# Kernel tuning notes

Hardware: AMD Instinct MI355X
Metric: run time of the kernel (lower is better)

The kernel has to match this reference:

```python
import jax, jax.numpy as jnp
import numpy as np

TEMPERATURE = 0.1  # matches init kwarg


def _l2_normalize(x):
    # tf.math.l2_normalize along axis=1
    return x / jnp.sqrt(jnp.sum(x * x, axis=1, keepdims=True))


def _nearest_neighbour(p, queue):
    # brute-force top-1 retrieval: [B,D] @ [D,Q] -> argmax -> gather
    sims = p @ queue.T                      # [B, Q]
    nn = queue[jnp.argmax(sims, axis=1)]    # [B, D]
    return p + jax.lax.stop_gradient(nn - p)


def setup_inputs() -> dict:
    key = jax.random.key(0)
    k1, k2, k3 = jax.random.split(key, 3)
    B, Q, D = 4096, 32768, 128
    return {
        "projections_1": jax.random.normal(k1, (B, D), dtype=jnp.float32),
        "projections_2": jax.random.normal(k2, (B, D), dtype=jnp.float32),
        "feature_queue": _l2_normalize(jax.random.normal(k3, (Q, D), dtype=jnp.float32)),
    }


def reference(projections_1, projections_2, feature_queue):
    p1 = _l2_normalize(projections_1)
    p2 = _l2_normalize(projections_2)
    n1 = _nearest_neighbour(p1, feature_queue)
    n2 = _nearest_neighbour(p2, feature_queue)
    t = TEMPERATURE
    s_1_2_1 = (n1 @ p2.T) / t   # [B, B]
    s_1_2_2 = (p2 @ n1.T) / t
    s_2_1_1 = (n2 @ p1.T) / t
    s_2_1_2 = (p1 @ n2.T) / t
    logits = jnp.concatenate([s_1_2_1, s_1_2_2, s_2_1_1, s_2_1_2], axis=0)  # [4B, B]
    B = p1.shape[0]
    labels = jnp.tile(jnp.arange(B), 4)  # [4B]
    log_probs = jax.nn.log_softmax(logits, axis=1)
    # sparse categorical crossentropy per row (from_logits=True)
    loss = -jnp.take_along_axis(log_probs, labels[:, None], axis=1)[:, 0]
    return loss
```

## Files before the change

kernel.cpp:

```cpp
#include <hip/hip_runtime.h>
#include <math.h>


#define B_N 4096
#define D_N 128
#define NP 8192
#define NTILE 512
#define INV_T 10.0f
#define C1F (10.0f * 1.4426950408889634f)
#define C2F (16.0f * 1.4426950408889634f)
#define W_WIN 8e-3f

typedef _Float16 half8 __attribute__((ext_vector_type(8)));
typedef __fp16 fp16x2 __attribute__((ext_vector_type(2)));
typedef float f32x4 __attribute__((ext_vector_type(4)));
union H8 { half8 v; fp16x2 h2[4]; };

#define OFF_PH 0u
#define OFF_QH 2097152u
#define OFF_NH 10485760u
#define OFF_TV 12582912u
#define OFF_RM1 20971520u
#define OFF_RM 21233664u
#define OFF_KEY 21266432u
#define OFF_DG 21331968u
#define OFF_SP 21364736u

__device__ __forceinline__ void gload16(const void* g, void* l) {
  __builtin_amdgcn_global_load_lds((const __attribute__((address_space(1))) void*)g,
                                   (__attribute__((address_space(3))) void*)l, 16, 0, 0);
}

__global__ __launch_bounds__(256) void k_normalize(const float* __restrict__ in1,
                                                   const float* __restrict__ in2,
                                                   _Float16* __restrict__ Ph) {
  int t = threadIdx.x, w = t >> 6, l = t & 63;
  int g = blockIdx.x * 4 + w;
  int view = g >> 12, row = g & (B_N - 1);
  const float* src = (view ? in2 : in1) + (size_t)row * D_N;
  float2 v = *(const float2*)(src + 2 * l);
  float ss = fmaf(v.x, v.x, v.y * v.y);
#pragma unroll
  for (int m = 1; m < 64; m <<= 1) ss += __shfl_xor(ss, m);
  float rn = 1.0f / sqrtf(ss);
  *(fp16x2*)(Ph + (size_t)g * D_N + 2 * l) = __builtin_amdgcn_cvt_pkrtz(v.x * rn, v.y * rn);
}

__global__ __launch_bounds__(256) void k_qcvt(const float* __restrict__ src,
                                              _Float16* __restrict__ dst) {
  int i = blockIdx.x * 256 + threadIdx.x;
  const float* s = src + (size_t)i * 8;
  float4 x = *(const float4*)s;
  float4 y = *(const float4*)(s + 4);
  H8 h;
  h.h2[0] = __builtin_amdgcn_cvt_pkrtz(x.x, x.y);
  h.h2[1] = __builtin_amdgcn_cvt_pkrtz(x.z, x.w);
  h.h2[2] = __builtin_amdgcn_cvt_pkrtz(y.x, y.y);
  h.h2[3] = __builtin_amdgcn_cvt_pkrtz(y.z, y.w);
  *(half8*)(dst + (size_t)i * 8) = h.v;
}

#define STAGE128(MAT, RB, BUF)                                                 \
  {                                                                            \
    _Pragma("unroll") for (int j = 0; j < 8; ++j) {                            \
      int ch = w * 8 + j;                                                      \
      int r = (ch << 2) + l4;                                                  \
      gload16(MAT + (((RB) + r) << 7) + ((l15 ^ (r & 7)) << 3),                \
              (char*)(&sm[BUF][0]) + (ch << 10));                              \
    }                                                                          \
  }

__global__ __launch_bounds__(256, 2) void k_nn(const _Float16* __restrict__ Qh,
                                               const _Float16* __restrict__ Ph,
                                               _Float16* __restrict__ tv) {
  __shared__ _Float16 sm[2][16384];
  int bid = blockIdx.x;
  int qc = (bid & 7) | ((bid >> 9) << 3);
  int pb = (bid >> 3) & 63;
  int t = threadIdx.x, l = t & 63, w = t >> 6;
  int wq = w >> 1, wp = w & 1, l15 = l & 15, l4 = l >> 4;
  half8 Pf4[4][4];
  const _Float16* pbase = Ph + (size_t)(pb * 128 + wp * 64 + l15) * D_N + l4 * 8;
#pragma unroll
  for (int tj = 0; tj < 4; ++tj)
#pragma unroll
    for (int ks = 0; ks < 4; ++ks)
      Pf4[tj][ks] = *(const half8*)(pbase + (size_t)tj * 16 * D_N + ks * 32);
  const size_t qrow0 = (size_t)qc * 2048;
  int tidb = qc * 32;
  int pcol = pb * 128 + wp * 64 + l15;
  STAGE128(Qh, qrow0, 0)
#pragma unroll 1
  for (int qt = 0; qt < 16; ++qt) {
    int cur = qt & 1;
    __syncthreads();
    if (qt < 15) STAGE128(Qh, qrow0 + (qt + 1) * 128, cur ^ 1)
    const char* bb = (const char*)(&sm[cur][0]);
    f32x4 acc[4][4];
#pragma unroll
    for (int i = 0; i < 4; ++i)
#pragma unroll
      for (int j = 0; j < 4; ++j) acc[i][j] = (f32x4){0.f, 0.f, 0.f, 0.f};
#pragma unroll
    for (int ks = 0; ks < 4; ++ks) {
      half8 Qf[4];
#pragma unroll
      for (int ti = 0; ti < 4; ++ti) {
        int qloc = wq * 64 + ti * 16 + l15;
        int byteo = qloc * 256 + ((((ks << 2) + l4) ^ (qloc & 7)) << 4);
        Qf[ti] = *(const half8*)(bb + byteo);
      }
#pragma unroll
      for (int ti = 0; ti < 4; ++ti)
#pragma unroll
        for (int tj = 0; tj < 4; ++tj)
          acc[ti][tj] =
              __builtin_amdgcn_mfma_f32_16x16x32_f16(Qf[ti], Pf4[tj][ks], acc[ti][tj], 0, 0, 0);
    }
    int tid = tidb + qt * 2 + wq;
#pragma unroll
    for (int tj = 0; tj < 4; ++tj) {
      float m = acc[0][tj][0];
#pragma unroll
      for (int ti = 0; ti < 4; ++ti)
#pragma unroll
        for (int r = 0; r < 4; ++r) m = fmaxf(m, acc[ti][tj][r]);
      m = fmaxf(m, __shfl_xor(m, 16));
      m = fmaxf(m, __shfl_xor(m, 32));
      if (l4 == 0) tv[(size_t)tid * NP + pcol + tj * 16] = (_Float16)m;
    }
  }
}

__global__ __launch_bounds__(256) void k_rowmax1(const _Float16* __restrict__ tv,
                                                 float* __restrict__ rm1) {
  int p = blockIdx.x * 256 + threadIdx.x;
  int g = blockIdx.y;
  float m = -3e38f;
  for (int tid = g * 64; tid < g * 64 + 64; ++tid) m = fmaxf(m, (float)tv[(size_t)tid * NP + p]);
  rm1[(size_t)g * NP + p] = m;
}

__global__ __launch_bounds__(256) void k_rowmax2(const float* __restrict__ rm1,
                                                 float* __restrict__ rowmax,
                                                 unsigned long long* __restrict__ keys) {
  int p = blockIdx.x * 256 + threadIdx.x;
  float m = rm1[p];
#pragma unroll
  for (int g = 1; g < 8; ++g) m = fmaxf(m, rm1[(size_t)g * NP + p]);
  rowmax[p] = m;
  keys[p] = 0ull;
}

__global__ __launch_bounds__(256) void k_rescore(const float* __restrict__ queue,
                                                 const float* __restrict__ in1,
                                                 const float* __restrict__ in2,
                                                 const _Float16* __restrict__ tv,
                                                 const float* __restrict__ rowmax,
                                                 unsigned long long* __restrict__ keys) {
  __shared__ float Qs[32][132];
  __shared__ unsigned short cand[NP];
  __shared__ int cnt;
  int tile = blockIdx.x, qh = blockIdx.y, t = threadIdx.x;
  if (t == 0) cnt = 0;
  __syncthreads();
  int qbase = tile * 64 + qh * 32;
#pragma unroll
  for (int j = 0; j < 4; ++j) {
    int i = j * 256 + t;
    int r = i >> 5, c = i & 31;
    *(float4*)(&Qs[r][c << 2]) = *(const float4*)(queue + ((size_t)(qbase + r) << 7) + (c << 2));
  }
  const _Float16* tvrow = tv + (size_t)tile * NP;
#pragma unroll
  for (int j = 0; j < 32; ++j) {
    int p = j * 256 + t;
    float v = (float)tvrow[p];
    if (v >= rowmax[p] - W_WIN) {
      int k = atomicAdd(&cnt, 1);
      cand[k] = (unsigned short)p;
    }
  }
  __syncthreads();
  int n = cnt;
  int w = t >> 6, l = t & 63, hl = l >> 5, ll = l & 31;
  for (int ci = w * 2 + hl; ci < n; ci += 8) {
    int p = cand[ci];
    const float* prow = (p < B_N) ? (in1 + ((size_t)p << 7)) : (in2 + ((size_t)(p - B_N) << 7));
    float d = 0.f;
#pragma unroll
    for (int k = 0; k < 32; ++k) {
      float4 a = *(const float4*)(prow + (k << 2));
      float4 b = *(const float4*)(&Qs[ll][k << 2]);
      d = fmaf(a.x, b.x, d);
      d = fmaf(a.y, b.y, d);
      d = fmaf(a.z, b.z, d);
      d = fmaf(a.w, b.w, d);
    }
    int idx = qbase + ll;
#pragma unroll
    for (int m = 1; m < 32; m <<= 1) {
      float ov = __shfl_xor(d, m);
      int oi = __shfl_xor(idx, m);
      if (ov > d || (ov == d && oi < idx)) {
        d = ov;
        idx = oi;
      }
    }
    if (ll == 0) {
      unsigned u = __float_as_uint(d);
      u = ((int)u < 0) ? ~u : (u | 0x80000000u);
      unsigned long long key = ((unsigned long long)u << 32) | (unsigned)(~idx);
      atomicMax(keys + p, key);
    }
  }
}

__global__ __launch_bounds__(256) void k_gather(const float* __restrict__ queue,
                                                const float* __restrict__ in1,
                                                const float* __restrict__ in2,
                                                const unsigned long long* __restrict__ keys,
                                                _Float16* __restrict__ Nh,
                                                float* __restrict__ diag) {
  int t = threadIdx.x, w = t >> 6, l = t & 63;
  int g = blockIdx.x * 4 + w;
  int view = g >> 12, row = g & (B_N - 1);
  unsigned long long key = keys[g];
  int qidx = (int)(~(unsigned)(key & 0xffffffffull));
  const float* q = queue + (size_t)qidx * D_N;
  float2 qv = *(const float2*)(q + 2 * l);
  *(fp16x2*)(Nh + (size_t)g * D_N + 2 * l) = __builtin_amdgcn_cvt_pkrtz(qv.x, qv.y);
  const float* oth = (view ? in1 : in2) + (size_t)row * D_N;
  float2 ov = *(const float2*)(oth + 2 * l);
  float ss = fmaf(ov.x, ov.x, ov.y * ov.y);
  float d = fmaf(qv.x, ov.x, qv.y * ov.y);
#pragma unroll
  for (int m = 1; m < 64; m <<= 1) {
    ss += __shfl_xor(ss, m);
    d += __shfl_xor(d, m);
  }
  if (l == 0) diag[g] = d / sqrtf(ss);
}

__global__ __launch_bounds__(256, 2) void k_loss(const _Float16* __restrict__ Ph,
                                                 const _Float16* __restrict__ Nh,
                                                 float* __restrict__ Spart) {
  __shared__ _Float16 sm[2][16384];
  __shared__ float sred[2][2][64];
  int rb = blockIdx.x;
  int chunk = blockIdx.y;
  int pair = rb >> 5, rowblk = rb & 31;
  const size_t BDh = (size_t)B_N * D_N;
  const _Float16* A = (pair == 0) ? Nh : (pair == 1) ? (Ph + BDh) : (pair == 2) ? (Nh + BDh) : Ph;
  const _Float16* Bm = (pair == 0) ? (Ph + BDh) : (pair == 1) ? Nh : (pair == 2) ? Ph : (Nh + BDh);
  int t = threadIdx.x, l = t & 63, w = t >> 6;
  int wr = w >> 1, wc = w & 1, l15 = l & 15, l4 = l >> 4;
  half8 Af[4][4];
  const _Float16* ab = A + (size_t)(rowblk * 128 + wr * 64 + l15) * D_N + l4 * 8;
#pragma unroll
  for (int ti = 0; ti < 4; ++ti)
#pragma unroll
    for (int ks = 0; ks < 4; ++ks)
      Af[ti][ks] = *(const half8*)(ab + (size_t)ti * 16 * D_N + ks * 32);
  float S[16];
#pragma unroll
  for (int i = 0; i < 16; ++i) S[i] = 0.f;
  const size_t crow0 = (size_t)chunk * 1024;
  STAGE128(Bm, crow0, 0)
#pragma unroll 1
  for (int ct = 0; ct < 8; ++ct) {
    int cur = ct & 1;
    __syncthreads();
    if (ct < 7) STAGE128(Bm, crow0 + (ct + 1) * 128, cur ^ 1)
    const char* bbp = (const char*)(&sm[cur][0]);
    f32x4 acc[4][4];
#pragma unroll
    for (int i = 0; i < 4; ++i)
#pragma unroll
      for (int j = 0; j < 4; ++j) acc[i][j] = (f32x4){0.f, 0.f, 0.f, 0.f};
#pragma unroll
    for (int ks = 0; ks < 4; ++ks) {
      half8 Bf[4];
#pragma unroll
      for (int tj = 0; tj < 4; ++tj) {
        int bloc = wc * 64 + tj * 16 + l15;
        int byteo = bloc * 256 + ((((ks << 2) + l4) ^ (bloc & 7)) << 4);
        Bf[tj] = *(const half8*)(bbp + byteo);
      }
#pragma unroll
      for (int ti = 0; ti < 4; ++ti)
#pragma unroll
        for (int tj = 0; tj < 4; ++tj)
          acc[ti][tj] =
              __builtin_amdgcn_mfma_f32_16x16x32_f16(Af[ti][ks], Bf[tj], acc[ti][tj], 0, 0, 0);
    }
#pragma unroll
    for (int ti = 0; ti < 4; ++ti)
#pragma unroll
      for (int r = 0; r < 4; ++r) {
        float e = 0.f;
#pragma unroll
        for (int tj = 0; tj < 4; ++tj) e += exp2f(fmaf(acc[ti][tj][r], C1F, -C2F));
        S[ti * 4 + r] += e;
      }
  }
#pragma unroll
  for (int i = 0; i < 16; ++i) {
#pragma unroll
    for (int m = 1; m < 16; m <<= 1) S[i] += __shfl_xor(S[i], m);
  }
  __syncthreads();
  if (l15 == 0) {
#pragma unroll
    for (int ti = 0; ti < 4; ++ti)
#pragma unroll
      for (int r = 0; r < 4; ++r) sred[wr][wc][ti * 16 + l4 * 4 + r] = S[ti * 4 + r];
  }
  __syncthreads();
  if (t < 128) {
    int wrr = t >> 6, rl = t & 63;
    float s = sred[wrr][0][rl] + sred[wrr][1][rl];
    int row = pair * B_N + rowblk * 128 + wrr * 64 + rl;
    Spart[(size_t)row * 4 + chunk] = s;
  }
}

__global__ __launch_bounds__(256) void k_merge(const float* __restrict__ Spart,
                                               const float* __restrict__ diag,
                                               float* __restrict__ out) {
  int row = blockIdx.x * 256 + threadIdx.x;
  const float* sp = Spart + (size_t)row * 4;
  float s = sp[0] + sp[1] + sp[2] + sp[3];
  int pair = row >> 12, r = row & (B_N - 1);
  float dg = diag[(pair >> 1) * B_N + r];
  out[row] = logf(s) + 16.0f - INV_T * dg;
}

extern "C" void kernel_launch(void* const* d_in, const int* in_sizes, int n_in,
                              void* d_out, int out_size, void* d_ws, size_t ws_size,
                              hipStream_t stream) {
  const float* in1 = (const float*)d_in[0];
  const float* in2 = (const float*)d_in[1];
  const float* queue = (const float*)d_in[2];
  float* out = (float*)d_out;
  char* ws = (char*)d_ws;
  _Float16* Ph = (_Float16*)(ws + OFF_PH);
  _Float16* Qhh = (_Float16*)(ws + OFF_QH);
  _Float16* Nh = (_Float16*)(ws + OFF_NH);
  _Float16* TV = (_Float16*)(ws + OFF_TV);
  float* RM1 = (float*)(ws + OFF_RM1);
  float* RM = (float*)(ws + OFF_RM);
  unsigned long long* KEY = (unsigned long long*)(ws + OFF_KEY);
  float* DG = (float*)(ws + OFF_DG);
  float* SP = (float*)(ws + OFF_SP);

  hipLaunchKernelGGL(k_normalize, dim3(2048), dim3(256), 0, stream, in1, in2, Ph);
  hipLaunchKernelGGL(k_qcvt, dim3(2048), dim3(256), 0, stream, queue, Qhh);
  hipLaunchKernelGGL(k_nn, dim3(1024), dim3(256), 0, stream, Qhh, Ph, TV);
  hipLaunchKernelGGL(k_rowmax1, dim3(32, 8), dim3(256), 0, stream, TV, RM1);
  hipLaunchKernelGGL(k_rowmax2, dim3(32), dim3(256), 0, stream, RM1, RM, KEY);
  hipLaunchKernelGGL(k_rescore, dim3(512, 2), dim3(256), 0, stream, queue, in1, in2, TV, RM, KEY);
  hipLaunchKernelGGL(k_gather, dim3(2048), dim3(256), 0, stream, queue, in1, in2, KEY, Nh, DG);
  hipLaunchKernelGGL(k_loss, dim3(128, 4), dim3(256), 0, stream, Ph, Nh, SP);
  hipLaunchKernelGGL(k_merge, dim3(64), dim3(256), 0, stream, SP, DG, out);
}
```

Measured before the change: 172.5 us.

## Halve MFMA tile depth, raise occupancy, use vmcnt-gated barriers, finer tile-max granularity

The NN and loss GEMM kernels now stage 64-row tiles instead of 128, halving LDS use and allowing 4 blocks per CU. Plain __syncthreads are replaced by explicit s_waitcnt vmcnt plus s_barrier, so the wait covers only the older tile while the next prefetch stays in flight. The NN kernel now writes per-32-row tile maxima, doubling the tile-value buffer. The rowmax and rescore stages are rescaled to match, and rescore reads candidates as vectorized half8/float4 loads. This trades more store and reduction traffic, plus more candidates to screen, for better latency hiding and occupancy.

```diff
diff --git a/kernel.cpp b/kernel.cpp
--- a/kernel.cpp
+++ b/kernel.cpp
@@ -5,7 +5,7 @@
 #define B_N 4096
 #define D_N 128
 #define NP 8192
-#define NTILE 512
+#define NT2 1024
 #define INV_T 10.0f
 #define C1F (10.0f * 1.4426950408889634f)
 #define C2F (16.0f * 1.4426950408889634f)
@@ -20,11 +20,18 @@
 #define OFF_QH 2097152u
 #define OFF_NH 10485760u
 #define OFF_TV 12582912u
-#define OFF_RM1 20971520u
-#define OFF_RM 21233664u
-#define OFF_KEY 21266432u
-#define OFF_DG 21331968u
-#define OFF_SP 21364736u
+#define OFF_RM1 29360128u
+#define OFF_RM 29884416u
+#define OFF_KEY 29917184u
+#define OFF_DG 29982720u
+#define OFF_SP 30015488u
+
+#define VMCNT(N) asm volatile("s_waitcnt vmcnt(" #N ")" ::: "memory")
+#define BARRIER()                      \
+  {                                    \
+    __builtin_amdgcn_s_barrier();      \
+    __builtin_amdgcn_sched_barrier(0); \
+  }
 
 __device__ __forceinline__ void gload16(const void* g, void* l) {
   __builtin_amdgcn_global_load_lds((const __attribute__((address_space(1))) void*)g,
@@ -60,20 +67,20 @@
   *(half8*)(dst + (size_t)i * 8) = h.v;
 }
 
-#define STAGE128(MAT, RB, BUF)                                                 \
+#define STAGE64(MAT, RB, BUF)                                                  \
   {                                                                            \
-    _Pragma("unroll") for (int j = 0; j < 8; ++j) {                            \
-      int ch = w * 8 + j;                                                      \
+    _Pragma("unroll") for (int j = 0; j < 4; ++j) {                            \
+      int ch = w * 4 + j;                                                      \
       int r = (ch << 2) + l4;                                                  \
       gload16(MAT + (((RB) + r) << 7) + ((l15 ^ (r & 7)) << 3),                \
               (char*)(&sm[BUF][0]) + (ch << 10));                              \
     }                                                                          \
   }
 
-__global__ __launch_bounds__(256, 2) void k_nn(const _Float16* __restrict__ Qh,
+__global__ __launch_bounds__(256, 4) void k_nn(const _Float16* __restrict__ Qh,
                                                const _Float16* __restrict__ Ph,
                                                _Float16* __restrict__ tv) {
-  __shared__ _Float16 sm[2][16384];
+  __shared__ _Float16 sm[2][8192];
   int bid = blockIdx.x;
   int qc = (bid & 7) | ((bid >> 9) << 3);
   int pb = (bid >> 3) & 63;
@@ -87,48 +94,53 @@
     for (int ks = 0; ks < 4; ++ks)
       Pf4[tj][ks] = *(const half8*)(pbase + (size_t)tj * 16 * D_N + ks * 32);
   const size_t qrow0 = (size_t)qc * 2048;
-  int tidb = qc * 32;
   int pcol = pb * 128 + wp * 64 + l15;
-  STAGE128(Qh, qrow0, 0)
+  STAGE64(Qh, qrow0, 0)
 #pragma unroll 1
-  for (int qt = 0; qt < 16; ++qt) {
-    int cur = qt & 1;
-    __syncthreads();
-    if (qt < 15) STAGE128(Qh, qrow0 + (qt + 1) * 128, cur ^ 1)
+  for (int s = 0; s < 32; ++s) {
+    int cur = s & 1;
+    if (s < 31) STAGE64(Qh, qrow0 + (size_t)(s + 1) * 64, cur ^ 1)
+    if (s == 0 || s == 31) {
+      VMCNT(4);
+    } else {
+      VMCNT(8);
+    }
+    BARRIER()
     const char* bb = (const char*)(&sm[cur][0]);
-    f32x4 acc[4][4];
-#pragma unroll
-    for (int i = 0; i < 4; ++i)
+    f32x4 acc[2][4];
+#pragma unroll
+    for (int i = 0; i < 2; ++i)
 #pragma unroll
       for (int j = 0; j < 4; ++j) acc[i][j] = (f32x4){0.f, 0.f, 0.f, 0.f};
 #pragma unroll
     for (int ks = 0; ks < 4; ++ks) {
-      half8 Qf[4];
-#pragma unroll
-      for (int ti = 0; ti < 4; ++ti) {
-        int qloc = wq * 64 + ti * 16 + l15;
+      half8 Qf[2];
+#pragma unroll
+      for (int ti = 0; ti < 2; ++ti) {
+        int qloc = wq * 32 + ti * 16 + l15;
         int byteo = qloc * 256 + ((((ks << 2) + l4) ^ (qloc & 7)) << 4);
         Qf[ti] = *(const half8*)(bb + byteo);
       }
 #pragma unroll
-      for (int ti = 0; ti < 4; ++ti)
+      for (int ti = 0; ti < 2; ++ti)
 #pragma unroll
         for (int tj = 0; tj < 4; ++tj)
           acc[ti][tj] =
               __builtin_amdgcn_mfma_f32_16x16x32_f16(Qf[ti], Pf4[tj][ks], acc[ti][tj], 0, 0, 0);
     }
-    int tid = tidb + qt * 2 + wq;
+    int tid2 = qc * 64 + s * 2 + wq;
 #pragma unroll
     for (int tj = 0; tj < 4; ++tj) {
       float m = acc[0][tj][0];
 #pragma unroll
-      for (int ti = 0; ti < 4; ++ti)
+      for (int ti = 0; ti < 2; ++ti)
 #pragma unroll
         for (int r = 0; r < 4; ++r) m = fmaxf(m, acc[ti][tj][r]);
       m = fmaxf(m, __shfl_xor(m, 16));
       m = fmaxf(m, __shfl_xor(m, 32));
-      if (l4 == 0) tv[(size_t)tid * NP + pcol + tj * 16] = (_Float16)m;
-    }
+      if (l4 == 0) tv[(size_t)tid2 * NP + pcol + tj * 16] = (_Float16)m;
+    }
+    BARRIER()
   }
 }
 
@@ -147,7 +159,7 @@
   int p = blockIdx.x * 256 + threadIdx.x;
   float m = rm1[p];
 #pragma unroll
-  for (int g = 1; g < 8; ++g) m = fmaxf(m, rm1[(size_t)g * NP + p]);
+  for (int g = 1; g < 16; ++g) m = fmaxf(m, rm1[(size_t)g * NP + p]);
   rowmax[p] = m;
   keys[p] = 0ull;
 }
@@ -161,10 +173,10 @@
   __shared__ float Qs[32][132];
   __shared__ unsigned short cand[NP];
   __shared__ int cnt;
-  int tile = blockIdx.x, qh = blockIdx.y, t = threadIdx.x;
+  int tile = blockIdx.x, t = threadIdx.x;
   if (t == 0) cnt = 0;
   __syncthreads();
-  int qbase = tile * 64 + qh * 32;
+  int qbase = tile << 5;
 #pragma unroll
   for (int j = 0; j < 4; ++j) {
     int i = j * 256 + t;
@@ -173,12 +185,18 @@
   }
   const _Float16* tvrow = tv + (size_t)tile * NP;
 #pragma unroll
-  for (int j = 0; j < 32; ++j) {
-    int p = j * 256 + t;
-    float v = (float)tvrow[p];
-    if (v >= rowmax[p] - W_WIN) {
-      int k = atomicAdd(&cnt, 1);
-      cand[k] = (unsigned short)p;
+  for (int j = 0; j < 4; ++j) {
+    int p0 = j * 2048 + t * 8;
+    half8 tvv = *(const half8*)(tvrow + p0);
+    float4 r0 = *(const float4*)(rowmax + p0);
+    float4 r1 = *(const float4*)(rowmax + p0 + 4);
+    float rm[8] = {r0.x, r0.y, r0.z, r0.w, r1.x, r1.y, r1.z, r1.w};
+#pragma unroll
+    for (int k = 0; k < 8; ++k) {
+      if ((float)tvv[k] >= rm[k] - W_WIN) {
+        int kk = atomicAdd(&cnt, 1);
+        cand[kk] = (unsigned short)(p0 + k);
+      }
     }
   }
   __syncthreads();
@@ -242,10 +260,10 @@
   if (l == 0) diag[g] = d / sqrtf(ss);
 }
 
-__global__ __launch_bounds__(256, 2) void k_loss(const _Float16* __restrict__ Ph,
+__global__ __launch_bounds__(256, 4) void k_loss(const _Float16* __restrict__ Ph,
                                                  const _Float16* __restrict__ Nh,
                                                  float* __restrict__ Spart) {
-  __shared__ _Float16 sm[2][16384];
+  __shared__ _Float16 sm[2][8192];
   __shared__ float sred[2][2][64];
   int rb = blockIdx.x;
   int chunk = blockIdx.y;
@@ -266,43 +284,46 @@
 #pragma unroll
   for (int i = 0; i < 16; ++i) S[i] = 0.f;
   const size_t crow0 = (size_t)chunk * 1024;
-  STAGE128(Bm, crow0, 0)
+  STAGE64(Bm, crow0, 0)
 #pragma unroll 1
-  for (int ct = 0; ct < 8; ++ct) {
+  for (int ct = 0; ct < 16; ++ct) {
     int cur = ct & 1;
-    __syncthreads();
-    if (ct < 7) STAGE128(Bm, crow0 + (ct + 1) * 128, cur ^ 1)
+    if (ct < 15) STAGE64(Bm, crow0 + (size_t)(ct + 1) * 64, cur ^ 1)
+    if (ct == 15) {
+      VMCNT(0);
+    } else {
+      VMCNT(4);
+    }
+    BARRIER()
     const char* bbp = (const char*)(&sm[cur][0]);
-    f32x4 acc[4][4];
+    f32x4 acc[4][2];
 #pragma unroll
     for (int i = 0; i < 4; ++i)
 #pragma unroll
-      for (int j = 0; j < 4; ++j) acc[i][j] = (f32x4){0.f, 0.f, 0.f, 0.f};
+      for (int j = 0; j < 2; ++j) acc[i][j] = (f32x4){0.f, 0.f, 0.f, 0.f};
 #pragma unroll
     for (int ks = 0; ks < 4; ++ks) {
-      half8 Bf[4];
-#pragma unroll
-      for (int tj = 0; tj < 4; ++tj) {
-        int bloc = wc * 64 + tj * 16 + l15;
+      half8 Bf[2];
+#pragma unroll
+      for (int tj = 0; tj < 2; ++tj) {
+        int bloc = wc * 32 + tj * 16 + l15;
         int byteo = bloc * 256 + ((((ks << 2) + l4) ^ (bloc & 7)) << 4);
         Bf[tj] = *(const half8*)(bbp + byteo);
       }
 #pragma unroll
       for (int ti = 0; ti < 4; ++ti)
 #pragma unroll
-        for (int tj = 0; tj < 4; ++tj)
+        for (int tj = 0; tj < 2; ++tj)
           acc[ti][tj] =
               __builtin_amdgcn_mfma_f32_16x16x32_f16(Af[ti][ks], Bf[tj], acc[ti][tj], 0, 0, 0);
     }
 #pragma unroll
     for (int ti = 0; ti < 4; ++ti)
 #pragma unroll
-      for (int r = 0; r < 4; ++r) {
-        float e = 0.f;
-#pragma unroll
-        for (int tj = 0; tj < 4; ++tj) e += exp2f(fmaf(acc[ti][tj][r], C1F, -C2F));
-        S[ti * 4 + r] += e;
-      }
+      for (int r = 0; r < 4; ++r)
+        S[ti * 4 + r] +=
+            exp2f(fmaf(acc[ti][0][r], C1F, -C2F)) + exp2f(fmaf(acc[ti][1][r], C1F, -C2F));
+    BARRIER()
   }
 #pragma unroll
   for (int i = 0; i < 16; ++i) {
@@ -357,9 +378,9 @@
   hipLaunchKernelGGL(k_normalize, dim3(2048), dim3(256), 0, stream, in1, in2, Ph);
   hipLaunchKernelGGL(k_qcvt, dim3(2048), dim3(256), 0, stream, queue, Qhh);
   hipLaunchKernelGGL(k_nn, dim3(1024), dim3(256), 0, stream, Qhh, Ph, TV);
-  hipLaunchKernelGGL(k_rowmax1, dim3(32, 8), dim3(256), 0, stream, TV, RM1);
+  hipLaunchKernelGGL(k_rowmax1, dim3(32, 16), dim3(256), 0, stream, TV, RM1);
   hipLaunchKernelGGL(k_rowmax2, dim3(32), dim3(256), 0, stream, RM1, RM, KEY);
-  hipLaunchKernelGGL(k_rescore, dim3(512, 2), dim3(256), 0, stream, queue, in1, in2, TV, RM, KEY);
+  hipLaunchKernelGGL(k_rescore, dim3(1024), dim3(256), 0, stream, queue, in1, in2, TV, RM, KEY);
   hipLaunchKernelGGL(k_gather, dim3(2048), dim3(256), 0, stream, queue, in1, in2, KEY, Nh, DG);
   hipLaunchKernelGGL(k_loss, dim3(128, 4), dim3(256), 0, stream, Ph, Nh, SP);
   hipLaunchKernelGGL(k_merge, dim3(64), dim3(256), 0, stream, SP, DG, out);
```

Result: slower. 193.5 us (+12.1%).

## Fuse prep kernels and compute row max via atomics in NN kernel

Applied to the files above, without the earlier changes.

Merges the normalize and queue-conversion kernels into one launch that also zeroes the key and row-max buffers. The per-column row maximum is now tracked in registers inside the NN kernel and published with an atomicMax on order-preserving packed floats. This removes the two row-max reduction kernels and their re-read of the tile-max buffer. The rescore candidate scan also switches to vectorized 8-wide loads. It costs some global atomics at the end of each NN block.

```diff
diff --git a/kernel.cpp b/kernel.cpp
--- a/kernel.cpp
+++ b/kernel.cpp
@@ -20,44 +20,58 @@
 #define OFF_QH 2097152u
 #define OFF_NH 10485760u
 #define OFF_TV 12582912u
-#define OFF_RM1 20971520u
-#define OFF_RM 21233664u
-#define OFF_KEY 21266432u
-#define OFF_DG 21331968u
-#define OFF_SP 21364736u
+#define OFF_RMU 20971520u
+#define OFF_KEY 21004288u
+#define OFF_DG 21069824u
+#define OFF_SP 21102592u
 
 __device__ __forceinline__ void gload16(const void* g, void* l) {
   __builtin_amdgcn_global_load_lds((const __attribute__((address_space(1))) void*)g,
                                    (__attribute__((address_space(3))) void*)l, 16, 0, 0);
 }
 
-__global__ __launch_bounds__(256) void k_normalize(const float* __restrict__ in1,
-                                                   const float* __restrict__ in2,
-                                                   _Float16* __restrict__ Ph) {
-  int t = threadIdx.x, w = t >> 6, l = t & 63;
-  int g = blockIdx.x * 4 + w;
-  int view = g >> 12, row = g & (B_N - 1);
-  const float* src = (view ? in2 : in1) + (size_t)row * D_N;
-  float2 v = *(const float2*)(src + 2 * l);
-  float ss = fmaf(v.x, v.x, v.y * v.y);
-#pragma unroll
-  for (int m = 1; m < 64; m <<= 1) ss += __shfl_xor(ss, m);
-  float rn = 1.0f / sqrtf(ss);
-  *(fp16x2*)(Ph + (size_t)g * D_N + 2 * l) = __builtin_amdgcn_cvt_pkrtz(v.x * rn, v.y * rn);
-}
-
-__global__ __launch_bounds__(256) void k_qcvt(const float* __restrict__ src,
-                                              _Float16* __restrict__ dst) {
-  int i = blockIdx.x * 256 + threadIdx.x;
-  const float* s = src + (size_t)i * 8;
-  float4 x = *(const float4*)s;
-  float4 y = *(const float4*)(s + 4);
-  H8 h;
-  h.h2[0] = __builtin_amdgcn_cvt_pkrtz(x.x, x.y);
-  h.h2[1] = __builtin_amdgcn_cvt_pkrtz(x.z, x.w);
-  h.h2[2] = __builtin_amdgcn_cvt_pkrtz(y.x, y.y);
-  h.h2[3] = __builtin_amdgcn_cvt_pkrtz(y.z, y.w);
-  *(half8*)(dst + (size_t)i * 8) = h.v;
+__device__ __forceinline__ unsigned packf(float f) {
+  unsigned u = __float_as_uint(f);
+  return ((int)u < 0) ? ~u : (u | 0x80000000u);
+}
+__device__ __forceinline__ float unpackf(unsigned p) {
+  unsigned v = (p & 0x80000000u) ? (p & 0x7fffffffu) : ~p;
+  return __uint_as_float(v);
+}
+
+__global__ __launch_bounds__(256) void k_prep(const float* __restrict__ in1,
+                                              const float* __restrict__ in2,
+                                              const float* __restrict__ queue,
+                                              _Float16* __restrict__ Ph,
+                                              _Float16* __restrict__ Qh,
+                                              unsigned long long* __restrict__ keys,
+                                              unsigned* __restrict__ rmu) {
+  int bid = blockIdx.x, t = threadIdx.x;
+  if (bid < 2048) {
+    int i = bid * 256 + t;
+    const float* s = queue + (size_t)i * 8;
+    float4 x = *(const float4*)s;
+    float4 y = *(const float4*)(s + 4);
+    H8 h;
+    h.h2[0] = __builtin_amdgcn_cvt_pkrtz(x.x, x.y);
+    h.h2[1] = __builtin_amdgcn_cvt_pkrtz(x.z, x.w);
+    h.h2[2] = __builtin_amdgcn_cvt_pkrtz(y.x, y.y);
+    h.h2[3] = __builtin_amdgcn_cvt_pkrtz(y.z, y.w);
+    *(half8*)(Qh + (size_t)i * 8) = h.v;
+  } else {
+    int w = t >> 6, l = t & 63;
+    int g = (bid - 2048) * 4 + w;
+    int view = g >> 12, row = g & (B_N - 1);
+    const float* src = (view ? in2 : in1) + (size_t)row * D_N;
+    float2 v = *(const float2*)(src + 2 * l);
+    float ss = fmaf(v.x, v.x, v.y * v.y);
+#pragma unroll
+    for (int m = 1; m < 64; m <<= 1) ss += __shfl_xor(ss, m);
+    float rn = 1.0f / sqrtf(ss);
+    *(fp16x2*)(Ph + (size_t)g * D_N + 2 * l) = __builtin_amdgcn_cvt_pkrtz(v.x * rn, v.y * rn);
+    if (l == 0) keys[g] = 0ull;
+    if (l == 1) rmu[g] = 0u;
+  }
 }
 
 #define STAGE128(MAT, RB, BUF)                                                 \
@@ -72,7 +86,8 @@
 
 __global__ __launch_bounds__(256, 2) void k_nn(const _Float16* __restrict__ Qh,
                                                const _Float16* __restrict__ Ph,
-                                               _Float16* __restrict__ tv) {
+                                               _Float16* __restrict__ tv,
+                                               unsigned* __restrict__ rmu) {
   __shared__ _Float16 sm[2][16384];
   int bid = blockIdx.x;
   int qc = (bid & 7) | ((bid >> 9) << 3);
@@ -89,6 +104,9 @@
   const size_t qrow0 = (size_t)qc * 2048;
   int tidb = qc * 32;
   int pcol = pb * 128 + wp * 64 + l15;
+  float runm[4];
+#pragma unroll
+  for (int tj = 0; tj < 4; ++tj) runm[tj] = -3e38f;
   STAGE128(Qh, qrow0, 0)
 #pragma unroll 1
   for (int qt = 0; qt < 16; ++qt) {
@@ -127,36 +145,21 @@
         for (int r = 0; r < 4; ++r) m = fmaxf(m, acc[ti][tj][r]);
       m = fmaxf(m, __shfl_xor(m, 16));
       m = fmaxf(m, __shfl_xor(m, 32));
+      runm[tj] = fmaxf(runm[tj], m);
       if (l4 == 0) tv[(size_t)tid * NP + pcol + tj * 16] = (_Float16)m;
     }
   }
-}
-
-__global__ __launch_bounds__(256) void k_rowmax1(const _Float16* __restrict__ tv,
-                                                 float* __restrict__ rm1) {
-  int p = blockIdx.x * 256 + threadIdx.x;
-  int g = blockIdx.y;
-  float m = -3e38f;
-  for (int tid = g * 64; tid < g * 64 + 64; ++tid) m = fmaxf(m, (float)tv[(size_t)tid * NP + p]);
-  rm1[(size_t)g * NP + p] = m;
-}
-
-__global__ __launch_bounds__(256) void k_rowmax2(const float* __restrict__ rm1,
-                                                 float* __restrict__ rowmax,
-                                                 unsigned long long* __restrict__ keys) {
-  int p = blockIdx.x * 256 + threadIdx.x;
-  float m = rm1[p];
-#pragma unroll
-  for (int g = 1; g < 8; ++g) m = fmaxf(m, rm1[(size_t)g * NP + p]);
-  rowmax[p] = m;
-  keys[p] = 0ull;
+  if (l4 == 0) {
+#pragma unroll
+    for (int tj = 0; tj < 4; ++tj) atomicMax(rmu + pcol + tj * 16, packf(runm[tj]));
+  }
 }
 
 __global__ __launch_bounds__(256) void k_rescore(const float* __restrict__ queue,
                                                  const float* __restrict__ in1,
                                                  const float* __restrict__ in2,
                                                  const _Float16* __restrict__ tv,
-                                                 const float* __restrict__ rowmax,
+                                                 const unsigned* __restrict__ rmu,
                                                  unsigned long long* __restrict__ keys) {
   __shared__ float Qs[32][132];
   __shared__ unsigned short cand[NP];
@@ -173,12 +176,18 @@
   }
   const _Float16* tvrow = tv + (size_t)tile * NP;
 #pragma unroll
-  for (int j = 0; j < 32; ++j) {
-    int p = j * 256 + t;
-    float v = (float)tvrow[p];
-    if (v >= rowmax[p] - W_WIN) {
-      int k = atomicAdd(&cnt, 1);
-      cand[k] = (unsigned short)p;
+  for (int j = 0; j < 4; ++j) {
+    int p0 = j * 2048 + t * 8;
+    half8 tvv = *(const half8*)(tvrow + p0);
+    uint4 u0 = *(const uint4*)(rmu + p0);
+    uint4 u1 = *(const uint4*)(rmu + p0 + 4);
+    unsigned uu[8] = {u0.x, u0.y, u0.z, u0.w, u1.x, u1.y, u1.z, u1.w};
+#pragma unroll
+    for (int k = 0; k < 8; ++k) {
+      if ((float)tvv[k] >= unpackf(uu[k]) - W_WIN) {
+        int pos = atomicAdd(&cnt, 1);
+        cand[pos] = (unsigned short)(p0 + k);
+      }
     }
   }
   __syncthreads();
@@ -208,9 +217,7 @@
       }
     }
     if (ll == 0) {
-      unsigned u = __float_as_uint(d);
-      u = ((int)u < 0) ? ~u : (u | 0x80000000u);
-      unsigned long long key = ((unsigned long long)u << 32) | (unsigned)(~idx);
+      unsigned long long key = ((unsigned long long)packf(d) << 32) | (unsigned)(~idx);
       atomicMax(keys + p, key);
     }
   }
@@ -348,18 +355,14 @@
   _Float16* Qhh = (_Float16*)(ws + OFF_QH);
   _Float16* Nh = (_Float16*)(ws + OFF_NH);
   _Float16* TV = (_Float16*)(ws + OFF_TV);
-  float* RM1 = (float*)(ws + OFF_RM1);
-  float* RM = (float*)(ws + OFF_RM);
+  unsigned* RMU = (unsigned*)(ws + OFF_RMU);
   unsigned long long* KEY = (unsigned long long*)(ws + OFF_KEY);
   float* DG = (float*)(ws + OFF_DG);
   float* SP = (float*)(ws + OFF_SP);
 
-  hipLaunchKernelGGL(k_normalize, dim3(2048), dim3(256), 0, stream, in1, in2, Ph);
-  hipLaunchKernelGGL(k_qcvt, dim3(2048), dim3(256), 0, stream, queue, Qhh);
-  hipLaunchKernelGGL(k_nn, dim3(1024), dim3(256), 0, stream, Qhh, Ph, TV);
-  hipLaunchKernelGGL(k_rowmax1, dim3(32, 8), dim3(256), 0, stream, TV, RM1);
-  hipLaunchKernelGGL(k_rowmax2, dim3(32), dim3(256), 0, stream, RM1, RM, KEY);
-  hipLaunchKernelGGL(k_rescore, dim3(512, 2), dim3(256), 0, stream, queue, in1, in2, TV, RM, KEY);
+  hipLaunchKernelGGL(k_prep, dim3(4096), dim3(256), 0, stream, in1, in2, queue, Ph, Qhh, KEY, RMU);
+  hipLaunchKernelGGL(k_nn, dim3(1024), dim3(256), 0, stream, Qhh, Ph, TV, RMU);
+  hipLaunchKernelGGL(k_rescore, dim3(512, 2), dim3(256), 0, stream, queue, in1, in2, TV, RMU, KEY);
   hipLaunchKernelGGL(k_gather, dim3(2048), dim3(256), 0, stream, queue, in1, in2, KEY, Nh, DG);
   hipLaunchKernelGGL(k_loss, dim3(128, 4), dim3(256), 0, stream, Ph, Nh, SP);
   hipLaunchKernelGGL(k_merge, dim3(64), dim3(256), 0, stream, SP, DG, out);
```

Measured after the change: 144.5 us (median of 2 runs). 1.19x faster.
